# Performance work log

Measured on AMD Instinct MI355X. Metric: run time of the kernel, lower is better.

The kernel has to match this reference:

```python
import jax, jax.numpy as jnp
import numpy as np
import math

B, T, D = 4, 2048, 1024
N, D_OUT = 1024, 1024
EPS_A = 1e-4
PROJ_BOUND = 1.0


def setup_inputs() -> dict:
    key = jax.random.key(0)
    ks = jax.random.split(key, 4)
    # reset_parameters: rho=0.99, delta0=1.0
    rho, delta0 = 0.99, 1.0
    alpha0 = -math.log(rho) / delta0
    alpha_log_val = math.log(math.expm1(alpha0))
    delta_bias_val = math.log(math.expm1(delta0))
    return {
        "u": jax.random.normal(ks[0], (B, T, D), dtype=jnp.float32),
        "z0": jnp.zeros((B, N), dtype=jnp.float32),
        "W_in_raw": 0.02 * jax.random.normal(ks[1], (N, D), dtype=jnp.float32),
        "W_out_raw": 0.02 * jax.random.normal(ks[2], (D_OUT, N), dtype=jnp.float32),
        "pn_w": 0.02 * jax.random.normal(ks[3], (3 * N, D), dtype=jnp.float32),
        "pn_b": jnp.zeros((3 * N,), dtype=jnp.float32),
        "alpha_log": jnp.full((N,), alpha_log_val, dtype=jnp.float32),
        "delta_bias": jnp.full((N,), delta_bias_val, dtype=jnp.float32),
        "log_gamma": jnp.float32(0.0),
    }


def _bounded_linear(x, W, bound):
    # y = x @ (W/scale)^T with ||W/scale||_2 <= bound (exact spectral norm)
    sigma = jnp.maximum(jnp.linalg.norm(W, ord=2), 1e-5)
    scale = jnp.maximum(sigma / bound, 1.0)
    return x @ (W / scale).T


def reference(u, z0, W_in_raw, W_out_raw, pn_w, pn_b, alpha_log, delta_bias, log_gamma):
    g = jnp.exp(log_gamma)
    u_scaled = g * _bounded_linear(u, W_in_raw, PROJ_BOUND)        # (B,T,N)
    raw = u @ pn_w.T + pn_b                                        # (B,T,3N)
    delta_raw, b_raw, c_raw = jnp.split(raw, 3, axis=-1)
    delta = jax.nn.softplus(delta_raw + delta_bias)
    alpha = jax.nn.softplus(alpha_log)                             # (N,)
    a = jnp.minimum(jnp.exp(-delta * alpha), 1.0 - EPS_A)          # (B,T,N)
    b = jnp.tanh(b_raw)
    c = jnp.tanh(c_raw)
    # exact spectral norm of [[a,b],[c,0]] per coordinate
    p = a * a + c * c
    r = b * b
    q = a * b
    disc = (p - r) * (p - r) + 4.0 * q * q
    lam_max = 0.5 * (p + r + jnp.sqrt(disc + 1e-12))
    sigma = jnp.sqrt(lam_max + 1e-12)
    scale = jnp.maximum(sigma, 1.0)
    a, b, c = a / scale, b / scale, c / scale
    # diagonal recurrence z_{t+1} = a_t * z_t + b_t * u_scaled_t via associative scan
    bu = b * u_scaled
    bu = bu.at[:, 0].add(a[:, 0] * z0)
    def combine(x, y):
        a1, b1 = x
        a2, b2 = y
        return (a2 * a1, a2 * b1 + b2)
    _, z_next = jax.lax.associative_scan(combine, (a, bu), axis=1)  # z_1..z_T (B,T,N)
    # y_t = W_out (c_t * z_t) with z_t = state BEFORE update (one-step delay)
    states = jnp.concatenate([z0[:, None, :], z_next[:, :-1, :]], axis=1)  # z_0..z_{T-1}
    y_hat = c * states
    y = _bounded_linear(y_hat, W_out_raw, PROJ_BOUND)              # (B,T,D_out)
    return y
```

## Files before the change

### kernel.cpp

```cpp
#include <hip/hip_runtime.h>
#include <stdint.h>

#define B_ 4
#define T_ 2048
#define D_ 1024
#define N_ 1024
#define TC 32
#define NCH (T_/TC)
#define SQN 8

typedef __attribute__((ext_vector_type(4))) float f32x4;
typedef __attribute__((ext_vector_type(8))) short bf16x8;
typedef __attribute__((ext_vector_type(4))) unsigned short us4;

__device__ __forceinline__ unsigned short f2bf(float f){
  unsigned int u = __float_as_uint(f);
  return (unsigned short)((u + 0x7fffu + ((u >> 16) & 1u)) >> 16);
}
__device__ __forceinline__ float bf2f(unsigned short h){
  return __uint_as_float(((unsigned int)h) << 16);
}

#define U4    2097152
#define WIN4   262144
#define PNW4   786432
#define WOUT4  262144
#define CONV_BLOCKS ((U4 + WIN4 + PNW4 + WOUT4 + 255)/256)

__global__ void k_convert_all(const float* __restrict__ u, const float* __restrict__ Win,
                              const float* __restrict__ pnw, const float* __restrict__ Wout,
                              unsigned short* __restrict__ u16, unsigned short* __restrict__ Wcat16,
                              unsigned short* __restrict__ Wout16, float* __restrict__ sc){
  if (blockIdx.x == 0 && threadIdx.x < 64) sc[threadIdx.x] = 0.f;
  long i = (long)blockIdx.x * 256 + threadIdx.x;
  const float* src; unsigned short* dst; long o;
  if (i < U4)                      { src = u;    dst = u16;               o = i; }
  else if (i < U4+WIN4)            { src = Win;  dst = Wcat16;            o = i - U4; }
  else if (i < U4+WIN4+PNW4)       { src = pnw;  dst = Wcat16 + 1048576;  o = i - (U4+WIN4); }
  else if (i < U4+WIN4+PNW4+WOUT4) { src = Wout; dst = Wout16;            o = i - (U4+WIN4+PNW4); }
  else return;
  float4 v = ((const float4*)src)[o];
  us4 w;
  w.x = f2bf(v.x); w.y = f2bf(v.y); w.z = f2bf(v.z); w.w = f2bf(v.w);
  ((us4*)dst)[o] = w;
}

__device__ __forceinline__ void load_lds16(const unsigned short* g, unsigned short* l){
  __builtin_amdgcn_global_load_lds((const __attribute__((address_space(1))) void*)g,
                                   (__attribute__((address_space(3))) void*)l, 16, 0, 0);
}

template<int OUTBF16>
__global__ __launch_bounds__(256) void k_gemm(
    const unsigned short* __restrict__ A,
    const unsigned short* __restrict__ Bmat,
    void* __restrict__ C0,
    int M, int N, int K,
    const float* __restrict__ sc, int step)
{
  __shared__ alignas(16) unsigned short As[128*64];
  __shared__ alignas(16) unsigned short Bs[128*64];
  const int tid = threadIdx.x;
  const int wid = tid >> 6;
  const int lane = tid & 63;
  const int bn = blockIdx.x, bm = blockIdx.y;

  char* C = (char*)C0;
  float outscale = (step >= 0) ? sc[step] : 1.f;

  const int wr = wid >> 1, wc = wid & 1;
  const int rg = lane >> 3;
  const int cby = (lane & 7) << 4;
  const int srow0 = wid * 32;
  const int frow = lane & 15;
  const int kgrp = lane >> 4;

  const size_t Abase = (size_t)bm * 128 * K;
  const size_t Bbase = (size_t)bn * 128 * K;

  f32x4 acc[4][4] = {};

  for (int kt = 0; kt < K; kt += 64){
    #pragma unroll
    for (int i = 0; i < 4; i++){
      int r = srow0 + i*8 + rg;
      int cb = cby ^ ((r & 7) << 4);
      load_lds16(A    + Abase + (size_t)r*K + kt + (cb >> 1), As + (srow0 + i*8)*64);
      load_lds16(Bmat + Bbase + (size_t)r*K + kt + (cb >> 1), Bs + (srow0 + i*8)*64);
    }
    __syncthreads();
    #pragma unroll
    for (int kk = 0; kk < 2; kk++){
      const int kbyte = kk*64 + kgrp*16;
      bf16x8 af[4], bfv[4];
      #pragma unroll
      for (int m = 0; m < 4; m++){
        int r = wr*64 + m*16 + frow;
        af[m] = *(const bf16x8*)((const char*)As + r*128 + (kbyte ^ ((r & 7) << 4)));
      }
      #pragma unroll
      for (int n2 = 0; n2 < 4; n2++){
        int r = wc*64 + n2*16 + frow;
        bfv[n2] = *(const bf16x8*)((const char*)Bs + r*128 + (kbyte ^ ((r & 7) << 4)));
      }
      #pragma unroll
      for (int m = 0; m < 4; m++)
        #pragma unroll
        for (int n2 = 0; n2 < 4; n2++)
          acc[m][n2] = __builtin_amdgcn_mfma_f32_16x16x32_bf16(af[m], bfv[n2], acc[m][n2], 0, 0, 0);
    }
    __syncthreads();
  }

  const int row0 = bm*128 + wr*64;
  const int col0 = bn*128 + wc*64 + frow;
  #pragma unroll
  for (int m = 0; m < 4; m++){
    #pragma unroll
    for (int n2 = 0; n2 < 4; n2++){
      const int col = col0 + n2*16;
      const int rb = row0 + m*16 + kgrp*4;
      #pragma unroll
      for (int j = 0; j < 4; j++){
        float v = acc[m][n2][j] * outscale;
        if (OUTBF16) ((unsigned short*)C)[(size_t)(rb + j)*N + col] = f2bf(v);
        else         ((float*)C)[(size_t)(rb + j)*N + col] = v;
      }
    }
  }
}

__global__ __launch_bounds__(256) void k_sq(
    const unsigned short* __restrict__ A0, unsigned short* __restrict__ C0,
    const unsigned short* __restrict__ A1, unsigned short* __restrict__ C1,
    float* __restrict__ sc, int step)
{
  __shared__ alignas(16) unsigned short As0[64*128], Bs0[64*128];
  __shared__ alignas(16) unsigned short As1[64*128], Bs1[64*128];
  const int tid = threadIdx.x;
  const int wid = tid >> 6;
  const int lane = tid & 63;
  const int bn = blockIdx.x, bm = blockIdx.y, z = blockIdx.z;

  const unsigned short* A = z ? A1 : A0;
  unsigned short* C = z ? C1 : C0;
  float outscale = 1.f;
  if (step > 0){ float t = sc[8 + (step-1)*2 + z]; outscale = 1.f/(t*t); }

  const int wr = wid >> 1, wc = wid & 1;
  const int frow = lane & 15;
  const int kgrp = lane >> 4;

  const int srl = lane >> 4;
  const int sgr = lane & 15;
  const int swzr = wid*4 + srl;
  const int scol_e = ((sgr ^ swzr) << 3);

  const size_t Arow = (size_t)bm * 64;
  const size_t Brow = (size_t)bn * 64;

  f32x4 acc[2][2] = {};

  auto stage = [&](unsigned short* as, unsigned short* bs, int t){
    const int kt = t * 128;
    #pragma unroll
    for (int i = 0; i < 4; i++){
      int r = i*16 + wid*4 + srl;
      load_lds16(A + (Arow + r)*1024 + kt + scol_e, as + (i*16 + wid*4)*128);
      load_lds16(A + (Brow + r)*1024 + kt + scol_e, bs + (i*16 + wid*4)*128);
    }
  };

  auto compute = [&](const unsigned short* as, const unsigned short* bs){
    #pragma unroll
    for (int ks = 0; ks < 4; ks++){
      const int kb = ks*64 + kgrp*16;
      bf16x8 af[2], bfv[2];
      #pragma unroll
      for (int m = 0; m < 2; m++){
        int r = wr*32 + m*16 + frow;
        af[m] = *(const bf16x8*)((const char*)as + r*256 + (kb ^ (frow << 4)));
      }
      #pragma unroll
      for (int n2 = 0; n2 < 2; n2++){
        int r = wc*32 + n2*16 + frow;
        bfv[n2] = *(const bf16x8*)((const char*)bs + r*256 + (kb ^ (frow << 4)));
      }
      #pragma unroll
      for (int m = 0; m < 2; m++)
        #pragma unroll
        for (int n2 = 0; n2 < 2; n2++)
          acc[m][n2] = __builtin_amdgcn_mfma_f32_16x16x32_bf16(af[m], bfv[n2], acc[m][n2], 0, 0, 0);
    }
  };

  stage(As0, Bs0, 0);
  __syncthreads();
  for (int t2 = 0; t2 < 8; t2 += 2){
    if (t2 + 1 < 8) stage(As1, Bs1, t2 + 1);
    compute(As0, Bs0);
    __syncthreads();
    if (t2 + 2 < 8) stage(As0, Bs0, t2 + 2);
    compute(As1, Bs1);
    __syncthreads();
  }

  const int row0 = bm*64 + wr*32;
  const int col0 = bn*64 + wc*32 + frow;
  float fr = 0.f;
  #pragma unroll
  for (int m = 0; m < 2; m++){
    #pragma unroll
    for (int n2 = 0; n2 < 2; n2++){
      const int col = col0 + n2*16;
      const int rb = row0 + m*16 + kgrp*4;
      #pragma unroll
      for (int j = 0; j < 4; j++){
        float v = acc[m][n2][j] * outscale;
        C[(size_t)(rb + j)*1024 + col] = f2bf(v);
        fr += v*v;
      }
    }
  }
  if (bm == bn && wr == wc){
    int j = frow - kgrp*4;
    if (j >= 0 && j < 4){
      float d = (acc[0][0][j] + acc[1][1][j]) * outscale;
      atomicAdd(&sc[8 + step*2 + z], d);
    }
  }
  if (step == SQN){
    #pragma unroll
    for (int off = 32; off; off >>= 1) fr += __shfl_down(fr, off, 64);
    if (lane == 0) atomicAdd(&sc[8 + 2*(SQN+1) + z], fr);
  }
}

__global__ void k_final(float* sc){
  int z = threadIdx.x;
  if (z < 2){
    float ll = 0.f, w = 1.f, t = 1.f;
    for (int i = 0; i <= SQN; i++){
      t = sc[8 + 2*i + z];
      ll += w * __logf(t);
      w *= 0.5f;
    }
    float tlast = sc[8 + 2*(SQN+1) + z] / (t*t);
    ll += w * __logf(tlast);
    float sig = __expf(0.5f * ll);
    sig = fmaxf(sig, 1e-5f);
    sc[z] = 1.f / fmaxf(sig, 1.f);
  }
}

__device__ __forceinline__ float softplusf(float x){
  return (x > 0.f) ? (x + __logf(1.f + __expf(-x))) : __logf(1.f + __expf(x));
}
__device__ __forceinline__ float tanhfastf(float x){
  float e = __expf(2.f * x);
  return 1.f - 2.f/(e + 1.f);
}
__device__ __forceinline__ void abc_from(float pin, float draw, float braw, float craw,
    float alpha, float ginv, float& a_o, float& bu_o, float& c_o){
  float sp = softplusf(draw);
  float av = __expf(-sp * alpha);
  av = fminf(av, 1.f - 1e-4f);
  float bv = tanhfastf(braw);
  float cv = tanhfastf(craw);
  float p = av*av + cv*cv;
  float r = bv*bv;
  float q = av*bv;
  float pr = p - r;
  float disc = pr*pr + 4.f*q*q;
  float lam = 0.5f*(p + r + sqrtf(disc + 1e-12f));
  float sig = sqrtf(lam + 1e-12f);
  float inv = 1.f / fmaxf(sig, 1.f);
  a_o = av * inv;
  c_o = cv * inv;
  bu_o = (bv * inv) * (pin * ginv);
}

__global__ __launch_bounds__(256) void k_pass1(
    const unsigned short* __restrict__ P,
    const float* __restrict__ alog, const float* __restrict__ dbias,
    const float* __restrict__ pnb, const float* __restrict__ lgam,
    const float* __restrict__ sc,
    float* __restrict__ Asum, float* __restrict__ Ssum)
{
  const int tid = threadIdx.x;
  const int n0 = blockIdx.y*512 + tid*2;
  const int ch = blockIdx.x, b = blockIdx.z;
  const float ginv = __expf(lgam[0]) * sc[0];
  float alpha[2], bd[2], bb[2], bc[2], A[2], S[2];
  #pragma unroll
  for (int j = 0; j < 2; j++){
    alpha[j] = softplusf(alog[n0+j]);
    bd[j] = dbias[n0+j] + pnb[n0+j];
    bb[j] = pnb[N_ + n0+j];
    bc[j] = pnb[2*N_ + n0+j];
    A[j] = 1.f; S[j] = 0.f;
  }
  const unsigned short* Pr = P + (size_t)(b*T_ + ch*TC) * (4*N_);
  #pragma unroll 4
  for (int i = 0; i < TC; i++){
    unsigned int vp = *(const unsigned int*)(Pr + n0);
    unsigned int vd = *(const unsigned int*)(Pr + N_ + n0);
    unsigned int vb = *(const unsigned int*)(Pr + 2*N_ + n0);
    unsigned int vc = *(const unsigned int*)(Pr + 3*N_ + n0);
    #pragma unroll
    for (int j = 0; j < 2; j++){
      float pin  = bf2f((unsigned short)(j ? (vp>>16) : (vp & 0xffffu)));
      float draw = bf2f((unsigned short)(j ? (vd>>16) : (vd & 0xffffu))) + bd[j];
      float braw = bf2f((unsigned short)(j ? (vb>>16) : (vb & 0xffffu))) + bb[j];
      float craw = bf2f((unsigned short)(j ? (vc>>16) : (vc & 0xffffu))) + bc[j];
      float a, bu, c;
      abc_from(pin, draw, braw, craw, alpha[j], ginv, a, bu, c);
      S[j] = fmaf(a, S[j], bu);
      A[j] *= a;
    }
    Pr += 4*N_;
  }
  const size_t idx = (size_t)(b*NCH + ch)*N_ + n0;
  Asum[idx] = A[0]; Asum[idx+1] = A[1];
  Ssum[idx] = S[0]; Ssum[idx+1] = S[1];
}

__global__ void k_pass2(const float* __restrict__ Asum, const float* __restrict__ Ssum,
                        const float* __restrict__ z0, float* __restrict__ Zent)
{
  const int n = blockIdx.x*256 + threadIdx.x;
  const int b = blockIdx.y;
  float z = z0[b*N_ + n];
  for (int ch = 0; ch < NCH; ch++){
    const size_t idx = (size_t)(b*NCH + ch)*N_ + n;
    Zent[idx] = z;
    z = fmaf(Asum[idx], z, Ssum[idx]);
  }
}

__global__ __launch_bounds__(256) void k_pass3(
    const unsigned short* __restrict__ P,
    const float* __restrict__ alog, const float* __restrict__ dbias,
    const float* __restrict__ pnb, const float* __restrict__ lgam,
    const float* __restrict__ sc, const float* __restrict__ Zent,
    unsigned short* __restrict__ yh)
{
  const int tid = threadIdx.x;
  const int n0 = blockIdx.y*512 + tid*2;
  const int ch = blockIdx.x, b = blockIdx.z;
  const float ginv = __expf(lgam[0]) * sc[0];
  float alpha[2], bd[2], bb[2], bc[2], z[2];
  #pragma unroll
  for (int j = 0; j < 2; j++){
    alpha[j] = softplusf(alog[n0+j]);
    bd[j] = dbias[n0+j] + pnb[n0+j];
    bb[j] = pnb[N_ + n0+j];
    bc[j] = pnb[2*N_ + n0+j];
  }
  const size_t zidx = (size_t)(b*NCH + ch)*N_ + n0;
  z[0] = Zent[zidx]; z[1] = Zent[zidx+1];
  const unsigned short* Pr = P + (size_t)(b*T_ + ch*TC) * (4*N_);
  unsigned short* Y = yh + (size_t)(b*T_ + ch*TC)*N_ + n0;
  #pragma unroll 4
  for (int i = 0; i < TC; i++){
    unsigned int vp = *(const unsigned int*)(Pr + n0);
    unsigned int vd = *(const unsigned int*)(Pr + N_ + n0);
    unsigned int vb = *(const unsigned int*)(Pr + 2*N_ + n0);
    unsigned int vc = *(const unsigned int*)(Pr + 3*N_ + n0);
    unsigned int ow = 0;
    #pragma unroll
    for (int j = 0; j < 2; j++){
      float pin  = bf2f((unsigned short)(j ? (vp>>16) : (vp & 0xffffu)));
      float draw = bf2f((unsigned short)(j ? (vd>>16) : (vd & 0xffffu))) + bd[j];
      float braw = bf2f((unsigned short)(j ? (vb>>16) : (vb & 0xffffu))) + bb[j];
      float craw = bf2f((unsigned short)(j ? (vc>>16) : (vc & 0xffffu))) + bc[j];
      float a, bu, c;
      abc_from(pin, draw, braw, craw, alpha[j], ginv, a, bu, c);
      float yv = c * z[j];
      z[j] = fmaf(a, z[j], bu);
      ow |= ((unsigned int)f2bf(yv)) << (16*j);
    }
    *(unsigned int*)Y = ow;
    Y += N_;
    Pr += 4*N_;
  }
}

extern "C" void kernel_launch(void* const* d_in, const int* in_sizes, int n_in,
                              void* d_out, int out_size, void* d_ws, size_t ws_size,
                              hipStream_t stream)
{
  const float* u    = (const float*)d_in[0];
  const float* z0   = (const float*)d_in[1];
  const float* Win  = (const float*)d_in[2];
  const float* Wout = (const float*)d_in[3];
  const float* pnw  = (const float*)d_in[4];
  const float* pnb  = (const float*)d_in[5];
  const float* alog = (const float*)d_in[6];
  const float* dbias= (const float*)d_in[7];
  const float* lgam = (const float*)d_in[8];

  char* ws = (char*)d_ws;
  size_t off = 0;
  auto alloc = [&](size_t bytes) -> void* {
    void* p = ws + off;
    off += (bytes + 255) & ~(size_t)255;
    return p;
  };
  float*          sc     = (float*)         alloc(1024);
  unsigned short* u16    = (unsigned short*)alloc((size_t)8192*1024*2);
  unsigned short* Wcat16 = (unsigned short*)alloc((size_t)4096*1024*2);
  unsigned short* Wout16 = (unsigned short*)alloc((size_t)1024*1024*2);
  unsigned short* P16    = (unsigned short*)alloc((size_t)8192*4096*2);
  unsigned short* yh16   = (unsigned short*)alloc((size_t)8192*1024*2);
  unsigned short* Hping  = (unsigned short*)alloc((size_t)2*1024*1024*2);
  unsigned short* Hpong  = (unsigned short*)alloc((size_t)2*1024*1024*2);
  float*          Asum   = (float*)alloc((size_t)B_*NCH*N_*4);
  float*          Ssum   = (float*)alloc((size_t)B_*NCH*N_*4);
  float*          Zent   = (float*)alloc((size_t)B_*NCH*N_*4);

  k_convert_all<<<CONV_BLOCKS, 256, 0, stream>>>(u, Win, pnw, Wout, u16, Wcat16, Wout16, sc);

  dim3 gsq(16, 16, 2);
  k_sq<<<gsq, 256, 0, stream>>>(Wcat16, Hping, Wout16, Hping + (size_t)1024*1024, sc, 0);
  unsigned short* hin = Hping;
  unsigned short* hout = Hpong;
  for (int s = 1; s <= SQN; s++){
    k_sq<<<gsq, 256, 0, stream>>>(hin, hout, hin + (size_t)1024*1024, hout + (size_t)1024*1024, sc, s);
    unsigned short* t = hin; hin = hout; hout = t;
  }
  k_final<<<1, 64, 0, stream>>>(sc);

  dim3 g1(4096/128, 8192/128, 1);
  k_gemm<1><<<g1, 256, 0, stream>>>(u16, Wcat16, P16, 8192, 4096, 1024, sc, -1);

  dim3 gp1(NCH, N_/512, B_);
  k_pass1<<<gp1, 256, 0, stream>>>(P16, alog, dbias, pnb, lgam, sc, Asum, Ssum);
  dim3 gp2(N_/256, B_);
  k_pass2<<<gp2, 256, 0, stream>>>(Asum, Ssum, z0, Zent);
  k_pass3<<<gp1, 256, 0, stream>>>(P16, alog, dbias, pnb, lgam, sc, Zent, yh16);

  dim3 g2(1024/128, 8192/128, 1);
  k_gemm<0><<<g2, 256, 0, stream>>>(yh16, Wout16, d_out, 8192, 1024, 1024, sc, 1);
}
```

Baseline: 320.9 us.

## Triple-buffer GEMM with larger tiles, fold spectral scale inline, cut one squaring step

Replaces the single-buffered 128x128 GEMM with a 256x128-tile, 512-thread kernel that prefetches two K-tiles ahead into a three-stage LDS ring. It uses precomputed LDS offsets, explicit waitcnt/barrier control and raised wave priority around the MFMA burst, aiming to hide global-load latency. The separate k_final launch is removed and the spectral-norm scale is recomputed inline in each consumer. The power-iteration squaring count drops from 8 to 7, which saves one launch but may loosen the accuracy of the spectral norm estimate.

```diff
diff --git a/kernel.cpp b/kernel.cpp
--- a/kernel.cpp
+++ b/kernel.cpp
@@ -7,7 +7,7 @@
 #define N_ 1024
 #define TC 32
 #define NCH (T_/TC)
-#define SQN 8
+#define SQN 7
 
 typedef __attribute__((ext_vector_type(4))) float f32x4;
 typedef __attribute__((ext_vector_type(8))) short bf16x8;
@@ -19,6 +19,20 @@
 }
 __device__ __forceinline__ float bf2f(unsigned short h){
   return __uint_as_float(((unsigned int)h) << 16);
+}
+
+__device__ __forceinline__ float inv_scale(const float* __restrict__ sc, int z){
+  float ll = 0.f, w = 1.f, t = 1.f;
+  #pragma unroll
+  for (int i = 0; i <= SQN; i++){
+    t = sc[8 + 2*i + z];
+    ll += w * __logf(t);
+    w *= 0.5f;
+  }
+  float F = sc[8 + 2*(SQN+1) + z];
+  ll += w * __logf(F / (t*t));
+  float sig = fmaxf(__expf(0.5f * ll), 1e-5f);
+  return 1.f / fmaxf(sig, 1.f);
 }
 
 #define U4    2097152
@@ -50,79 +64,119 @@
                                    (__attribute__((address_space(3))) void*)l, 16, 0, 0);
 }
 
-template<int OUTBF16>
-__global__ __launch_bounds__(256) void k_gemm(
+template<int OUTBF16, int ZSC>
+__global__ __launch_bounds__(512, 2) void k_big(
     const unsigned short* __restrict__ A,
     const unsigned short* __restrict__ Bmat,
     void* __restrict__ C0,
-    int M, int N, int K,
-    const float* __restrict__ sc, int step)
-{
-  __shared__ alignas(16) unsigned short As[128*64];
-  __shared__ alignas(16) unsigned short Bs[128*64];
+    int N, const float* __restrict__ sc)
+{
+  __shared__ alignas(16) unsigned short As3[3][256*64];
+  __shared__ alignas(16) unsigned short Bs3[3][128*64];
   const int tid = threadIdx.x;
   const int wid = tid >> 6;
   const int lane = tid & 63;
   const int bn = blockIdx.x, bm = blockIdx.y;
 
-  char* C = (char*)C0;
-  float outscale = (step >= 0) ? sc[step] : 1.f;
-
-  const int wr = wid >> 1, wc = wid & 1;
-  const int rg = lane >> 3;
-  const int cby = (lane & 7) << 4;
-  const int srow0 = wid * 32;
+  const int wr = wid >> 1;
+  const int wc = wid & 1;
   const int frow = lane & 15;
   const int kgrp = lane >> 4;
 
-  const size_t Abase = (size_t)bm * 128 * K;
-  const size_t Bbase = (size_t)bn * 128 * K;
+  const float outscale = (ZSC >= 0) ? inv_scale(sc, ZSC) : 1.f;
+
+  const unsigned short* Ab = A + (size_t)bm * 256 * 1024;
+  const unsigned short* Bb = Bmat + (size_t)bn * 128 * 1024;
+
+  int aoff[4][2], boff[4][2];
+  #pragma unroll
+  for (int m = 0; m < 4; m++){
+    int r = wr*64 + m*16 + frow;
+    #pragma unroll
+    for (int ks = 0; ks < 2; ks++)
+      aoff[m][ks] = r*128 + ((ks*64 + kgrp*16) ^ ((r & 7) << 4));
+  }
+  #pragma unroll
+  for (int n = 0; n < 4; n++){
+    int r = wc*64 + n*16 + frow;
+    #pragma unroll
+    for (int ks = 0; ks < 2; ks++)
+      boff[n][ks] = r*128 + ((ks*64 + kgrp*16) ^ ((r & 7) << 4));
+  }
 
   f32x4 acc[4][4] = {};
 
-  for (int kt = 0; kt < K; kt += 64){
-    #pragma unroll
-    for (int i = 0; i < 4; i++){
-      int r = srow0 + i*8 + rg;
-      int cb = cby ^ ((r & 7) << 4);
-      load_lds16(A    + Abase + (size_t)r*K + kt + (cb >> 1), As + (srow0 + i*8)*64);
-      load_lds16(Bmat + Bbase + (size_t)r*K + kt + (cb >> 1), Bs + (srow0 + i*8)*64);
-    }
-    __syncthreads();
-    #pragma unroll
-    for (int kk = 0; kk < 2; kk++){
-      const int kbyte = kk*64 + kgrp*16;
-      bf16x8 af[4], bfv[4];
-      #pragma unroll
-      for (int m = 0; m < 4; m++){
-        int r = wr*64 + m*16 + frow;
-        af[m] = *(const bf16x8*)((const char*)As + r*128 + (kbyte ^ ((r & 7) << 4)));
-      }
-      #pragma unroll
-      for (int n2 = 0; n2 < 4; n2++){
-        int r = wc*64 + n2*16 + frow;
-        bfv[n2] = *(const bf16x8*)((const char*)Bs + r*128 + (kbyte ^ ((r & 7) << 4)));
-      }
+  auto stage = [&](int t){
+    const int p = t % 3;
+    #pragma unroll
+    for (int l = 0; l < 4; l++){
+      int gi = l*512 + tid;
+      int r = gi >> 3;
+      int cb = (gi & 7) << 4;
+      int colel = t*64 + (((cb ^ ((r & 7) << 4))) >> 1);
+      load_lds16(Ab + (size_t)r*1024 + colel, &As3[p][gi*8]);
+    }
+    #pragma unroll
+    for (int l = 0; l < 2; l++){
+      int gi = l*512 + tid;
+      int r = gi >> 3;
+      int cb = (gi & 7) << 4;
+      int colel = t*64 + (((cb ^ ((r & 7) << 4))) >> 1);
+      load_lds16(Bb + (size_t)r*1024 + colel, &Bs3[p][gi*8]);
+    }
+  };
+
+  stage(0); stage(1);
+  asm volatile("s_waitcnt vmcnt(6)" ::: "memory");
+  __builtin_amdgcn_s_barrier();
+
+  for (int t = 0; t < 16; ++t){
+    if (t < 14) stage(t + 2);
+    const int p = t % 3;
+    const char* ab = (const char*)&As3[p][0];
+    const char* bb = (const char*)&Bs3[p][0];
+    bf16x8 af[4][2], bfv[4][2];
+    #pragma unroll
+    for (int m = 0; m < 4; m++)
+      #pragma unroll
+      for (int ks = 0; ks < 2; ks++)
+        af[m][ks] = *(const bf16x8*)(ab + aoff[m][ks]);
+    #pragma unroll
+    for (int n = 0; n < 4; n++)
+      #pragma unroll
+      for (int ks = 0; ks < 2; ks++)
+        bfv[n][ks] = *(const bf16x8*)(bb + boff[n][ks]);
+    asm volatile("s_waitcnt lgkmcnt(0)" ::: "memory");
+    __builtin_amdgcn_sched_barrier(0);
+    __builtin_amdgcn_s_setprio(1);
+    #pragma unroll
+    for (int ks = 0; ks < 2; ks++)
       #pragma unroll
       for (int m = 0; m < 4; m++)
         #pragma unroll
-        for (int n2 = 0; n2 < 4; n2++)
-          acc[m][n2] = __builtin_amdgcn_mfma_f32_16x16x32_bf16(af[m], bfv[n2], acc[m][n2], 0, 0, 0);
-    }
-    __syncthreads();
-  }
-
-  const int row0 = bm*128 + wr*64;
+        for (int n = 0; n < 4; n++)
+          acc[m][n] = __builtin_amdgcn_mfma_f32_16x16x32_bf16(af[m][ks], bfv[n][ks], acc[m][n], 0, 0, 0);
+    __builtin_amdgcn_s_setprio(0);
+    __builtin_amdgcn_sched_barrier(0);
+    if (t < 15){
+      if (t < 14) asm volatile("s_waitcnt vmcnt(6)" ::: "memory");
+      else        asm volatile("s_waitcnt vmcnt(0)" ::: "memory");
+      __builtin_amdgcn_s_barrier();
+    }
+  }
+
+  const int row0 = bm*256 + wr*64;
   const int col0 = bn*128 + wc*64 + frow;
+  char* C = (char*)C0;
   #pragma unroll
   for (int m = 0; m < 4; m++){
     #pragma unroll
-    for (int n2 = 0; n2 < 4; n2++){
-      const int col = col0 + n2*16;
+    for (int n = 0; n < 4; n++){
+      const int col = col0 + n*16;
       const int rb = row0 + m*16 + kgrp*4;
       #pragma unroll
       for (int j = 0; j < 4; j++){
-        float v = acc[m][n2][j] * outscale;
+        float v = acc[m][n][j] * outscale;
         if (OUTBF16) ((unsigned short*)C)[(size_t)(rb + j)*N + col] = f2bf(v);
         else         ((float*)C)[(size_t)(rb + j)*N + col] = v;
       }
@@ -233,23 +287,6 @@
     #pragma unroll
     for (int off = 32; off; off >>= 1) fr += __shfl_down(fr, off, 64);
     if (lane == 0) atomicAdd(&sc[8 + 2*(SQN+1) + z], fr);
-  }
-}
-
-__global__ void k_final(float* sc){
-  int z = threadIdx.x;
-  if (z < 2){
-    float ll = 0.f, w = 1.f, t = 1.f;
-    for (int i = 0; i <= SQN; i++){
-      t = sc[8 + 2*i + z];
-      ll += w * __logf(t);
-      w *= 0.5f;
-    }
-    float tlast = sc[8 + 2*(SQN+1) + z] / (t*t);
-    ll += w * __logf(tlast);
-    float sig = __expf(0.5f * ll);
-    sig = fmaxf(sig, 1e-5f);
-    sc[z] = 1.f / fmaxf(sig, 1.f);
   }
 }
 
@@ -290,7 +327,7 @@
   const int tid = threadIdx.x;
   const int n0 = blockIdx.y*512 + tid*2;
   const int ch = blockIdx.x, b = blockIdx.z;
-  const float ginv = __expf(lgam[0]) * sc[0];
+  const float ginv = __expf(lgam[0]) * inv_scale(sc, 0);
   float alpha[2], bd[2], bb[2], bc[2], A[2], S[2];
   #pragma unroll
   for (int j = 0; j < 2; j++){
@@ -348,7 +385,7 @@
   const int tid = threadIdx.x;
   const int n0 = blockIdx.y*512 + tid*2;
   const int ch = blockIdx.x, b = blockIdx.z;
-  const float ginv = __expf(lgam[0]) * sc[0];
+  const float ginv = __expf(lgam[0]) * inv_scale(sc, 0);
   float alpha[2], bd[2], bb[2], bc[2], z[2];
   #pragma unroll
   for (int j = 0; j < 2; j++){
@@ -429,10 +466,9 @@
     k_sq<<<gsq, 256, 0, stream>>>(hin, hout, hin + (size_t)1024*1024, hout + (size_t)1024*1024, sc, s);
     unsigned short* t = hin; hin = hout; hout = t;
   }
-  k_final<<<1, 64, 0, stream>>>(sc);
-
-  dim3 g1(4096/128, 8192/128, 1);
-  k_gemm<1><<<g1, 256, 0, stream>>>(u16, Wcat16, P16, 8192, 4096, 1024, sc, -1);
+
+  dim3 g1(4096/128, 8192/256);
+  k_big<1, -1><<<g1, 512, 0, stream>>>(u16, Wcat16, P16, 4096, sc);
 
   dim3 gp1(NCH, N_/512, B_);
   k_pass1<<<gp1, 256, 0, stream>>>(P16, alog, dbias, pnb, lgam, sc, Asum, Ssum);
@@ -440,6 +476,6 @@
   k_pass2<<<gp2, 256, 0, stream>>>(Asum, Ssum, z0, Zent);
   k_pass3<<<gp1, 256, 0, stream>>>(P16, alog, dbias, pnb, lgam, sc, Zent, yh16);
 
-  dim3 g2(1024/128, 8192/128, 1);
-  k_gemm<0><<<g2, 256, 0, stream>>>(yh16, Wout16, d_out, 8192, 1024, 1024, sc, 1);
-}
+  dim3 g2(1024/128, 8192/256);
+  k_big<0, 1><<<g2, 512, 0, stream>>>(yh16, Wout16, d_out, 1024, sc);
+}
```

Measured after the change: 326.0 us. No clear change (+1.6%).
